# Performance work log

Measured on AMD Instinct MI355X. Metric: run time of the kernel, lower is better.

## Reference

```python
import jax, jax.numpy as jnp
import numpy as np

ALPHA = 0.2  # LeakyReLU negative slope
EPS = 1e-6


def gam(x):
    # relu6(x+3)/3 + eps
    return jnp.clip(x + 3.0, 0.0, 6.0) / 3.0 + EPS


def leaky(x):
    return jnp.where(x >= 0, x, ALPHA * x)


def relu_bt(x):
    # threshold at detached inf-norm of input: min(leaky_relu(x), ||x||_inf)
    t = jax.lax.stop_gradient(jnp.max(jnp.abs(x)))
    return jnp.minimum(leaky(x), t)


def setup_inputs() -> dict:
    key = jax.random.key(0)
    ks = jax.random.split(key, 8)
    N, E, Din, Dout = 100000, 1600000, 256, 64
    return {
        "input": jax.random.normal(ks[0], (N, Din), dtype=jnp.float32),
        "edge": jax.random.randint(ks[1], (2, E), 0, N, dtype=jnp.int32),
        "W_high": jax.random.normal(ks[2], (Din, Dout), dtype=jnp.float32) * 0.06,
        "W_low": jax.random.normal(ks[3], (Din, Dout), dtype=jnp.float32) * 0.06,
        "a_high": jax.random.normal(ks[4], (1, 4 * Dout), dtype=jnp.float32) * 0.09,
        "a_low": jax.random.normal(ks[5], (1, 4 * Dout), dtype=jnp.float32) * 0.09,
        "c_high": jax.random.uniform(ks[6], (1, 1), dtype=jnp.float32),
        "c_low": jax.random.uniform(ks[7], (1, 1), dtype=jnp.float32),
    }


def reference(input, edge, W_high, W_low, a_high, a_low, c_high, c_low):
    N = input.shape[0]
    F = W_high.shape[1]
    src, dst = edge[0], edge[1]

    theta_high = gam(c_high) / 2.0  # [1,1]
    theta_low = gam(c_low) / 2.0

    h_high = relu_bt(input @ W_high)  # [N,F]
    h_low = relu_bt(input @ W_low)

    hh_s, hh_d = h_high[src], h_high[dst]  # [E,F]
    hl_s, hl_d = h_low[src], h_low[dst]

    ah = a_high[0]
    al = a_low[0]
    # a . [h_i, h_j, h_i+h_j, h_i-h_j] folded into per-endpoint coefficients
    # NOTE: original code uses h_high for the first two blocks of the LOW branch too.
    score_high = hh_s @ (ah[:F] + ah[2 * F:3 * F] + ah[3 * F:]) \
               + hh_d @ (ah[F:2 * F] + ah[2 * F:3 * F] - ah[3 * F:])  # [E]
    score_low = hh_s @ al[:F] + hh_d @ al[F:2 * F] \
              + hl_s @ (al[2 * F:3 * F] + al[3 * F:]) \
              + hl_d @ (al[2 * F:3 * F] - al[3 * F:])

    e_high = jnp.exp(-leaky(score_high / jnp.linalg.norm(a_high)))  # [E]
    e_low = jnp.exp(-leaky(score_low / jnp.linalg.norm(a_low)))

    # sparse COO spmm: rowsum and weighted aggregation
    rowsum_high = jax.ops.segment_sum(e_high, src, num_segments=N)[:, None]  # [N,1]
    rowsum_low = jax.ops.segment_sum(e_low, src, num_segments=N)[:, None]
    hp_high = jax.ops.segment_sum(e_high[:, None] * hh_d, src, num_segments=N)  # [N,F]
    hp_low = jax.ops.segment_sum(e_low[:, None] * hl_d, src, num_segments=N)

    hp_high = hp_high / (rowsum_high + theta_high)
    hp_low = hp_low / (rowsum_low + theta_low)

    # concat=True branch
    return relu_bt(jnp.concatenate([hp_high, hp_low], axis=1))  # [N,2F]
```

## Files before the change

kernel.cpp:

```cpp
#include <hip/hip_runtime.h>
#include <hip/hip_bf16.h>
#include <hip/hip_fp16.h>
#include <math.h>

typedef unsigned short ushort_t;
typedef unsigned int uint_t;
typedef __attribute__((ext_vector_type(8))) short short8;
typedef __attribute__((ext_vector_type(4))) float floatx4;
typedef __attribute__((ext_vector_type(4))) uint_t uintx4;

#define ALPHA 0.2f
#define CAP 64

__device__ __forceinline__ float leaky(float x) { return x >= 0.0f ? x : ALPHA * x; }

__device__ __forceinline__ float bf2f(ushort_t u) {
    union { uint_t i; float f; } v; v.i = ((uint_t)u) << 16; return v.f;
}
__device__ __forceinline__ ushort_t f2bf(float f) {
    union { float f; uint_t i; } v; v.f = f;
    return (ushort_t)((v.i + 0x8000u) >> 16);
}
__device__ __forceinline__ uint_t pack_bf2(float a, float b) {
    union { float f; uint_t i; } ua, ub; ua.f = a; ub.f = b;
    return ((ua.i + 0x8000u) >> 16) | ((ub.i + 0x8000u) & 0xffff0000u);
}

__global__ void prep_wtrans_kernel(const float* __restrict__ Wh, const float* __restrict__ Wl,
                                   ushort_t* __restrict__ WTg,
                                   const float* __restrict__ ah, const float* __restrict__ al,
                                   const float* __restrict__ ch, const float* __restrict__ cl,
                                   float* __restrict__ coef, float* __restrict__ consts) {
    int t = threadIdx.x;
    if (blockIdx.x < 128) {
        int c = blockIdx.x;
        float v = (c < 64) ? Wh[t * 64 + c] : Wl[t * 64 + (c - 64)];
        WTg[c * 256 + t] = f2bf(v);
        return;
    }
    __shared__ float red[256];
    float va = ah[t];
    red[t] = va * va;
    __syncthreads();
    for (int s = 128; s > 0; s >>= 1) { if (t < s) red[t] += red[t + s]; __syncthreads(); }
    float sum_h = red[0];
    __syncthreads();
    float vb = al[t];
    red[t] = vb * vb;
    __syncthreads();
    for (int s = 128; s > 0; s >>= 1) { if (t < s) red[t] += red[t + s]; __syncthreads(); }
    float sum_l = red[0];

    if (t == 0) {
        consts[0] = 1.0f / sqrtf(sum_h);
        consts[1] = 1.0f / sqrtf(sum_l);
        float c = ch[0];
        float g = fminf(fmaxf(c + 3.0f, 0.0f), 6.0f) / 3.0f + 1e-6f;
        consts[2] = g * 0.5f;
        c = cl[0];
        g = fminf(fmaxf(c + 3.0f, 0.0f), 6.0f) / 3.0f + 1e-6f;
        consts[3] = g * 0.5f;
    }
    if (t < 128) {
        int f = t;
        float c0, c1, c2, c3;
        if (f < 64) {
            c0 = ah[f] + ah[128 + f] + ah[192 + f];
            c1 = ah[64 + f] + ah[128 + f] - ah[192 + f];
            c2 = al[f];
            c3 = al[64 + f];
        } else {
            int g = f - 64;
            c0 = 0.0f;
            c1 = 0.0f;
            c2 = al[128 + g] + al[192 + g];
            c3 = al[128 + g] - al[192 + g];
        }
        coef[0 * 128 + f] = c0;
        coef[1 * 128 + f] = c1;
        coef[2 * 128 + f] = c2;
        coef[3 * 128 + f] = c3;
    }
}

__global__ __launch_bounds__(256, 4) void gemm_kernel(const float* __restrict__ in,
                                                      const ushort_t* __restrict__ WTg,
                                                      const float* __restrict__ coef,
                                                      ushort_t* __restrict__ hcat,
                                                      float* __restrict__ s4, int N) {
    __shared__ ushort_t WT[128 * 128];
    __shared__ float coefS[512];
    int tid = threadIdx.x;
    for (int i = tid; i < 512; i += 256) coefS[i] = coef[i];

    int wave = tid >> 6, lane = tid & 63;
    int quad = lane >> 4, m16 = lane & 15;
    int rowbase = blockIdx.x * 64 + wave * 16;
    int arow = rowbase + m16;
    if (arow >= N) arow = N - 1;

    floatx4 acc[8];
#pragma unroll
    for (int ct = 0; ct < 8; ++ct) acc[ct] = (floatx4){0.0f, 0.0f, 0.0f, 0.0f};

    const uint4* WTg4 = (const uint4*)WTg;

#pragma unroll
    for (int kh = 0; kh < 2; ++kh) {
        if (kh) __syncthreads();
        for (int i = tid; i < 2048; i += 256) {
            int c = i >> 4, j = i & 15;
            int sj = j ^ (c & 7);
            uint4 v = WTg4[c * 32 + kh * 16 + j];
            *(uint4*)&WT[c * 128 + sj * 8] = v;
        }
        __syncthreads();
#pragma unroll
        for (int ks = 0; ks < 4; ++ks) {
            const float* ap = in + (size_t)arow * 256 + kh * 128 + ks * 32 + quad * 8;
            float4 a0 = *(const float4*)ap;
            float4 a1 = *(const float4*)(ap + 4);
            union { uintx4 u; short8 s; } av;
            av.u[0] = pack_bf2(a0.x, a0.y);
            av.u[1] = pack_bf2(a0.z, a0.w);
            av.u[2] = pack_bf2(a1.x, a1.y);
            av.u[3] = pack_bf2(a1.z, a1.w);
#pragma unroll
            for (int ct = 0; ct < 8; ++ct) {
                int c = ct * 16 + m16;
                int sch = (ks * 4 + quad) ^ (c & 7);
                short8 b = *(const short8*)&WT[c * 128 + sch * 8];
                acc[ct] = __builtin_amdgcn_mfma_f32_16x16x32_bf16(av.s, b, acc[ct], 0, 0, 0);
            }
        }
    }

    float hv[8][4];
#pragma unroll
    for (int ct = 0; ct < 8; ++ct) {
#pragma unroll
        for (int r = 0; r < 4; ++r) {
            int row = rowbase + quad * 4 + r;
            float v = leaky(acc[ct][r]);
            hv[ct][r] = v;
            if (row < N) hcat[(size_t)row * 128 + ct * 16 + m16] = f2bf(v);
        }
    }
#pragma unroll
    for (int r = 0; r < 4; ++r) {
        int row = rowbase + quad * 4 + r;
        float p0 = 0, p1 = 0, p2 = 0, p3 = 0;
#pragma unroll
        for (int ct = 0; ct < 8; ++ct) {
            int c = ct * 16 + m16;
            float h = hv[ct][r];
            p0 += coefS[c] * h;
            p1 += coefS[128 + c] * h;
            p2 += coefS[256 + c] * h;
            p3 += coefS[384 + c] * h;
        }
#pragma unroll
        for (int off = 1; off < 16; off <<= 1) {
            p0 += __shfl_xor(p0, off);
            p1 += __shfl_xor(p1, off);
            p2 += __shfl_xor(p2, off);
            p3 += __shfl_xor(p3, off);
        }
        if (m16 == 0 && row < N) {
            floatx4 v = {p0, p1, p2, p3};
            *(floatx4*)&s4[(size_t)row * 4] = v;
        }
    }
}

__global__ void scatter_kernel(const int* __restrict__ edge, const float* __restrict__ s4,
                               const float* __restrict__ consts, int* __restrict__ cursor,
                               uint2* __restrict__ elist, int E) {
    int e = blockIdx.x * blockDim.x + threadIdx.x;
    if (e >= E) return;
    int src = edge[e];
    int dst = edge[E + e];
    float4 ss = *(const float4*)&s4[(size_t)src * 4];
    float4 sd = *(const float4*)&s4[(size_t)dst * 4];
    float eh = __expf(-leaky((ss.x + sd.y) * consts[0]));
    float el = __expf(-leaky((ss.z + sd.w) * consts[1]));
    int pos = atomicAdd(&cursor[src], 1);
    if (pos >= CAP) return;
    uint_t he = __half_as_ushort(__float2half(eh));
    uint_t hl = __half_as_ushort(__float2half(el));
    uint2 rec;
    rec.x = (uint_t)dst;
    rec.y = (uint_t)he | ((uint_t)hl << 16);
    elist[(size_t)src * CAP + pos] = rec;
}

__global__ __launch_bounds__(256) void aggregate_kernel(const int* __restrict__ deg,
                                                        const uint2* __restrict__ elist,
                                                        const ushort_t* __restrict__ hcat,
                                                        const float* __restrict__ consts,
                                                        float* __restrict__ out, int N) {
    int w = (blockIdx.x * blockDim.x + threadIdx.x) >> 6;
    int lane = threadIdx.x & 63;
    if (w >= N) return;
    int d = deg[w];
    if (d > CAP) d = CAP;
    int s = w * CAP;
    int e = s + d;
    bool hi = lane < 32;
    int wsh = hi ? 0 : 16;
    int col = lane * 2;

    float a0 = 0, a1 = 0, b0 = 0, b1 = 0;
    float sw0 = 0, sw1 = 0;

    int i = s;
    for (; i + 8 <= e; i += 8) {
        uint2 rr[8];
#pragma unroll
        for (int j = 0; j < 8; ++j) rr[j] = elist[i + j];
        uint_t pp[8];
#pragma unroll
        for (int j = 0; j < 8; ++j)
            pp[j] = *(const uint_t*)&hcat[(size_t)(int)rr[j].x * 128 + col];
#pragma unroll
        for (int j = 0; j < 8; ++j) {
            float wt = __half2float(__ushort_as_half((ushort_t)((rr[j].y >> wsh) & 0xffff)));
            float f0 = bf2f((ushort_t)(pp[j] & 0xffff));
            float f1 = bf2f((ushort_t)(pp[j] >> 16));
            if (j & 1) { b0 += wt * f0; b1 += wt * f1; sw1 += wt; }
            else       { a0 += wt * f0; a1 += wt * f1; sw0 += wt; }
        }
    }
    for (; i < e; ++i) {
        uint2 r = elist[i];
        uint_t p = *(const uint_t*)&hcat[(size_t)(int)r.x * 128 + col];
        float wt = __half2float(__ushort_as_half((ushort_t)((r.y >> wsh) & 0xffff)));
        a0 += wt * bf2f((ushort_t)(p & 0xffff));
        a1 += wt * bf2f((ushort_t)(p >> 16));
        sw0 += wt;
    }

    float acc0 = a0 + b0;
    float acc1 = a1 + b1;
    float rsum = sw0 + sw1;

    float theta = hi ? consts[2] : consts[3];
    float inv = 1.0f / (rsum + theta);
    float2 r;
    r.x = leaky(acc0 * inv);
    r.y = leaky(acc1 * inv);
    *(float2*)&out[(size_t)w * 128 + col] = r;
}

extern "C" void kernel_launch(void* const* d_in, const int* in_sizes, int n_in,
                              void* d_out, int out_size, void* d_ws, size_t ws_size,
                              hipStream_t stream) {
    const float* input = (const float*)d_in[0];
    const int* edge = (const int*)d_in[1];
    const float* Wh = (const float*)d_in[2];
    const float* Wl = (const float*)d_in[3];
    const float* ah = (const float*)d_in[4];
    const float* al = (const float*)d_in[5];
    const float* ch = (const float*)d_in[6];
    const float* cl = (const float*)d_in[7];
    int N = in_sizes[0] / 256;
    int E = in_sizes[1] / 2;
    float* out = (float*)d_out;

    char* ws = (char*)d_ws;
    size_t off = 0;
    uint2* elist = (uint2*)(ws + off);       off += (size_t)N * CAP * 8;
    ushort_t* hcat = (ushort_t*)(ws + off);  off += (size_t)N * 128 * 2;
    float* s4 = (float*)(ws + off);          off += (size_t)N * 4 * 4;
    int* cursor = (int*)(ws + off);          off += (size_t)N * 4;
    ushort_t* WTg = (ushort_t*)(ws + off);   off += 128 * 256 * 2;
    float* coef = (float*)(ws + off);        off += 4 * 128 * 4;
    float* consts = (float*)(ws + off);      off += 64;

    hipMemsetAsync(cursor, 0, (size_t)N * 4, stream);
    prep_wtrans_kernel<<<129, 256, 0, stream>>>(Wh, Wl, WTg, ah, al, ch, cl, coef, consts);
    gemm_kernel<<<(N + 63) / 64, 256, 0, stream>>>(input, WTg, coef, hcat, s4, N);
    scatter_kernel<<<(E + 255) / 256, 256, 0, stream>>>(edge, s4, consts, cursor, elist, E);
    aggregate_kernel<<<(N + 3) / 4, 256, 0, stream>>>(cursor, elist, hcat, consts, out, N);
}
```

Measured before the change: 375.4 us.

## Move edge weight computation into aggregate and partition scatter by XCD node ranges

The scatter kernel now only buckets destination indices, as 4-byte records instead of 8-byte ones. Blocks are assigned to XCDs, and each XCD handles only sources in its own node range, so the cursor atomics and elist writes stay local to that XCD's L2. The exponential edge weights are now computed in the aggregate kernel from the per-node scores s4, which costs one extra gathered float per edge per half-wave. In exchange it avoids reading s4 at scatter time and halves the elist traffic. The trade-off is that every block reads the full edge source array, about 8x more edge reads, and the grid-to-XCD mapping assumption may not hold.

```diff
diff --git a/kernel.cpp b/kernel.cpp
--- a/kernel.cpp
+++ b/kernel.cpp
@@ -11,6 +11,7 @@
 
 #define ALPHA 0.2f
 #define CAP 64
+#define NXCD 8
 
 __device__ __forceinline__ float leaky(float x) { return x >= 0.0f ? x : ALPHA * x; }
 
@@ -173,30 +174,31 @@
     }
 }
 
-__global__ void scatter_kernel(const int* __restrict__ edge, const float* __restrict__ s4,
-                               const float* __restrict__ consts, int* __restrict__ cursor,
-                               uint2* __restrict__ elist, int E) {
-    int e = blockIdx.x * blockDim.x + threadIdx.x;
-    if (e >= E) return;
-    int src = edge[e];
-    int dst = edge[E + e];
-    float4 ss = *(const float4*)&s4[(size_t)src * 4];
-    float4 sd = *(const float4*)&s4[(size_t)dst * 4];
-    float eh = __expf(-leaky((ss.x + sd.y) * consts[0]));
-    float el = __expf(-leaky((ss.z + sd.w) * consts[1]));
-    int pos = atomicAdd(&cursor[src], 1);
-    if (pos >= CAP) return;
-    uint_t he = __half_as_ushort(__float2half(eh));
-    uint_t hl = __half_as_ushort(__float2half(el));
-    uint2 rec;
-    rec.x = (uint_t)dst;
-    rec.y = (uint_t)he | ((uint_t)hl << 16);
-    elist[(size_t)src * CAP + pos] = rec;
+__global__ __launch_bounds__(256) void scatter_kernel(const int* __restrict__ edge,
+                                                      int* __restrict__ cursor,
+                                                      uint_t* __restrict__ elist,
+                                                      int E, int N) {
+    int xcd = blockIdx.x & (NXCD - 1);
+    int chunk = blockIdx.x >> 3;
+    int nchunks = gridDim.x >> 3;
+    int TN = (N + NXCD - 1) / NXCD;
+    int lo = xcd * TN;
+    int hiN = lo + TN;
+    int stride = nchunks * 256;
+    for (int e = chunk * 256 + threadIdx.x; e < E; e += stride) {
+        int src = edge[e];
+        if (src >= lo && src < hiN) {
+            int dst = edge[E + e];
+            int pos = atomicAdd(&cursor[src], 1);
+            if (pos < CAP) elist[(size_t)src * CAP + pos] = (uint_t)dst;
+        }
+    }
 }
 
 __global__ __launch_bounds__(256) void aggregate_kernel(const int* __restrict__ deg,
-                                                        const uint2* __restrict__ elist,
+                                                        const uint_t* __restrict__ elist,
                                                         const ushort_t* __restrict__ hcat,
+                                                        const float* __restrict__ s4,
                                                         const float* __restrict__ consts,
                                                         float* __restrict__ out, int N) {
     int w = (blockIdx.x * blockDim.x + threadIdx.x) >> 6;
@@ -207,24 +209,30 @@
     int s = w * CAP;
     int e = s + d;
     bool hi = lane < 32;
-    int wsh = hi ? 0 : 16;
     int col = lane * 2;
+
+    float inv_norm = hi ? consts[0] : consts[1];
+    float s_own = s4[(size_t)w * 4 + (hi ? 0 : 2)];
+    const float* s4o = s4 + (hi ? 1 : 3);
 
     float a0 = 0, a1 = 0, b0 = 0, b1 = 0;
     float sw0 = 0, sw1 = 0;
 
     int i = s;
     for (; i + 8 <= e; i += 8) {
-        uint2 rr[8];
+        uint_t rr[8];
 #pragma unroll
         for (int j = 0; j < 8; ++j) rr[j] = elist[i + j];
         uint_t pp[8];
-#pragma unroll
-        for (int j = 0; j < 8; ++j)
-            pp[j] = *(const uint_t*)&hcat[(size_t)(int)rr[j].x * 128 + col];
+        float so[8];
 #pragma unroll
         for (int j = 0; j < 8; ++j) {
-            float wt = __half2float(__ushort_as_half((ushort_t)((rr[j].y >> wsh) & 0xffff)));
+            so[j] = s4o[(size_t)rr[j] * 4];
+            pp[j] = *(const uint_t*)&hcat[(size_t)rr[j] * 128 + col];
+        }
+#pragma unroll
+        for (int j = 0; j < 8; ++j) {
+            float wt = __expf(-leaky((s_own + so[j]) * inv_norm));
             float f0 = bf2f((ushort_t)(pp[j] & 0xffff));
             float f1 = bf2f((ushort_t)(pp[j] >> 16));
             if (j & 1) { b0 += wt * f0; b1 += wt * f1; sw1 += wt; }
@@ -232,9 +240,10 @@
         }
     }
     for (; i < e; ++i) {
-        uint2 r = elist[i];
-        uint_t p = *(const uint_t*)&hcat[(size_t)(int)r.x * 128 + col];
-        float wt = __half2float(__ushort_as_half((ushort_t)((r.y >> wsh) & 0xffff)));
+        uint_t rec = elist[i];
+        float so = s4o[(size_t)rec * 4];
+        uint_t p = *(const uint_t*)&hcat[(size_t)rec * 128 + col];
+        float wt = __expf(-leaky((s_own + so) * inv_norm));
         a0 += wt * bf2f((ushort_t)(p & 0xffff));
         a1 += wt * bf2f((ushort_t)(p >> 16));
         sw0 += wt;
@@ -269,7 +278,7 @@
 
     char* ws = (char*)d_ws;
     size_t off = 0;
-    uint2* elist = (uint2*)(ws + off);       off += (size_t)N * CAP * 8;
+    uint_t* elist = (uint_t*)(ws + off);     off += (size_t)N * CAP * 4;
     ushort_t* hcat = (ushort_t*)(ws + off);  off += (size_t)N * 128 * 2;
     float* s4 = (float*)(ws + off);          off += (size_t)N * 4 * 4;
     int* cursor = (int*)(ws + off);          off += (size_t)N * 4;
@@ -280,6 +289,7 @@
     hipMemsetAsync(cursor, 0, (size_t)N * 4, stream);
     prep_wtrans_kernel<<<129, 256, 0, stream>>>(Wh, Wl, WTg, ah, al, ch, cl, coef, consts);
     gemm_kernel<<<(N + 63) / 64, 256, 0, stream>>>(input, WTg, coef, hcat, s4, N);
-    scatter_kernel<<<(E + 255) / 256, 256, 0, stream>>>(edge, s4, consts, cursor, elist, E);
-    aggregate_kernel<<<(N + 3) / 4, 256, 0, stream>>>(cursor, elist, hcat, consts, out, N);
-}
+    int nchunks = (E + 256 * 8 - 1) / (256 * 8);
+    scatter_kernel<<<nchunks * NXCD, 256, 0, stream>>>(edge, cursor, elist, E, N);
+    aggregate_kernel<<<(N + 3) / 4, 256, 0, stream>>>(cursor, elist, hcat, s4, consts, out, N);
+}
```

Result: no change. 369.1 us (-1.7%).
